# Kernel tuning notes

Measured on AMD Instinct MI355X. Metric: run time of the kernel, lower is better.

Reference implementation:

```python
import jax, jax.numpy as jnp
import numpy as np

N_HEADS = 16
BLOCK_SIZE = 256


def _rope(x):
    # x: [B, H, L, d] ; matches torch RotaryPositionalEmbedding (interleave-split then concat)
    B, H, L, d = x.shape
    inv_freq = 1.0 / (10000.0 ** (jnp.arange(0, d, 2, dtype=jnp.float32) / d))
    t = jnp.arange(L, dtype=jnp.float32)[:, None] * inv_freq[None, :]  # [L, d/2]
    cos, sin = jnp.cos(t), jnp.sin(t)
    x1, x2 = x[..., 0::2], x[..., 1::2]
    return jnp.concatenate([x1 * cos - x2 * sin, x2 * cos + x1 * sin], axis=-1)


def setup_inputs() -> dict:
    key = jax.random.key(0)
    k1, k2, k3 = jax.random.split(key, 3)
    B, L, D = 2, 4096, 1024
    x = jax.random.normal(k1, (B, L, D), dtype=jnp.float32)
    Wqkv = jax.random.normal(k2, (3 * D, D), dtype=jnp.float32) * 0.02
    Wout = jax.random.normal(k3, (D, D), dtype=jnp.float32) * 0.02
    return {"x": x, "Wqkv": Wqkv, "Wout": Wout}


def reference(x, Wqkv, Wout):
    H, BS = N_HEADS, BLOCK_SIZE
    B, L, D = x.shape
    HD = D // H
    scale = HD ** (-0.5)
    nb = L // BS

    qkv = (x @ Wqkv.T).reshape(B, L, 3, H, HD).transpose(2, 0, 3, 1, 4)  # [3,B,H,L,HD]
    q, k, v = qkv[0], qkv[1], qkv[2]
    q, k = _rope(q), _rope(k)

    # block-diagonal causal attention: only within-block scores are ever unmasked,
    # and fp32 exp(finfo.min - max) == 0, so blockwise softmax == masked full softmax
    qb = q.reshape(B, H, nb, BS, HD)
    kb = k.reshape(B, H, nb, BS, HD)
    vb = v.reshape(B, H, nb, BS, HD)

    att = jnp.einsum('bhnqd,bhnkd->bhnqk', qb, kb) * scale
    causal = jnp.tril(jnp.ones((BS, BS), dtype=bool))
    att = jnp.where(causal, att, jnp.finfo(att.dtype).min)
    att = jax.nn.softmax(att, axis=-1)  # dropout p=0.0 -> identity

    out = jnp.einsum('bhnqk,bhnkd->bhnqd', att, vb)
    out = out.reshape(B, H, L, HD).transpose(0, 2, 1, 3).reshape(B, L, D)
    return out @ Wout.T
```

## Files before the change

kernel.cpp:

```cpp
#include <hip/hip_runtime.h>
#include <hip/hip_bf16.h>
#include <cstdint>
#include <cstddef>

typedef __hip_bfloat16 bf16;
typedef __attribute__((ext_vector_type(8))) short bf16x8;
typedef __attribute__((ext_vector_type(4))) float floatx4;

static constexpr int Bb = 2;
static constexpr int Ls = 4096;
static constexpr int Dm = 1024;
static constexpr int Hn = 16;
static constexpr int HD = 64;
static constexpr int BS = 256;
static constexpr int QKVROW = 3 * Dm;
static constexpr int KRP = 72;

static constexpr size_t NX  = (size_t)8192 * 1024;
static constexpr size_t NQ  = (size_t)8192 * 3072;
static constexpr size_t NW1 = (size_t)3072 * 1024;
static constexpr size_t NW2 = (size_t)1024 * 1024;

__device__ __forceinline__ void async_load16(const void* g, void* l) {
  __builtin_amdgcn_global_load_lds(
      (__attribute__((address_space(1))) void*)(void*)(g),
      (__attribute__((address_space(3))) void*)(l), 16, 0, 0);
}

__device__ __forceinline__ short f2bf(float f) {
  union { __hip_bfloat16 b; short s; } u;
  u.b = __float2bfloat16(f);
  return u.s;
}

__device__ __forceinline__ float bf2f(short s) {
  union { unsigned u; float f; } v;
  v.u = ((unsigned)(unsigned short)s) << 16;
  return v.f;
}

__device__ __forceinline__ bf16x8 load8(const float* p) {
  const float4 f0 = *(const float4*)(const void*)p;
  const float4 f1 = *(const float4*)(const void*)(p + 4);
  bf16x8 r;
  r[0] = f2bf(f0.x); r[1] = f2bf(f0.y); r[2] = f2bf(f0.z); r[3] = f2bf(f0.w);
  r[4] = f2bf(f1.x); r[5] = f2bf(f1.y); r[6] = f2bf(f1.z); r[7] = f2bf(f1.w);
  return r;
}

__device__ __forceinline__ void storeC(bf16* C, size_t idx, float v) {
  C[idx] = __float2bfloat16(v);
}
__device__ __forceinline__ void storeC(float* C, size_t idx, float v) {
  C[idx] = v;
}

__global__ void cvt3_kernel(const float* __restrict__ x, const float* __restrict__ w1,
                            const float* __restrict__ w2, bf16* __restrict__ xb,
                            bf16* __restrict__ w1b, bf16* __restrict__ w2b) {
  const size_t i = ((size_t)blockIdx.x * 256 + threadIdx.x) * 8;
  if (i < NX) {
    *(bf16x8*)(void*)((short*)(void*)xb + i) = load8(x + i);
  } else if (i < NX + NW1) {
    const size_t k = i - NX;
    *(bf16x8*)(void*)((short*)(void*)w1b + k) = load8(w1 + k);
  } else {
    const size_t k = i - NX - NW1;
    *(bf16x8*)(void*)((short*)(void*)w2b + k) = load8(w2 + k);
  }
}

template <typename TC>
__global__ __launch_bounds__(512, 2) void gemm_sq(
    const bf16* __restrict__ A, const bf16* __restrict__ Bm, TC* __restrict__ C,
    int M, int N, int K) {
  constexpr int BK = 64;
  __shared__ __align__(16) short sA[2][2][128 * 64];
  __shared__ __align__(16) short sB[2][2][128 * 64];
  const int tid = threadIdx.x;
  const int wave = tid >> 6, lane = tid & 63;
  const int quad = lane >> 4, l15 = lane & 15;
  const int wr = wave >> 2, wc = wave & 3;
  const int tm = blockIdx.y * 256, tn = blockIdx.x * 256;

  const int iLo = tid >> 3;
  const int csP = tid & 7;
  const int csL = csP ^ (iLo & 7);
  const bf16* gA[2][2];
  const bf16* gB[2][2];
#pragma unroll
  for (int h = 0; h < 2; h++)
#pragma unroll
    for (int j = 0; j < 2; j++) {
      gA[h][j] = A + (size_t)(tm + h * 128 + iLo + 64 * j) * K + csL * 8;
      gB[h][j] = Bm + (size_t)(tn + h * 128 + iLo + 64 * j) * K + csL * 8;
    }

#define STGA(buf, h, kb)                                       \
  do {                                                         \
    short* d_ = &sA[buf][h][0] + tid * 8;                      \
    async_load16(gA[h][0] + (kb), d_);                         \
    async_load16(gA[h][1] + (kb), d_ + 4096);                  \
  } while (0)
#define STGB(buf, h, kb)                                       \
  do {                                                         \
    short* d_ = &sB[buf][h][0] + tid * 8;                      \
    async_load16(gB[h][0] + (kb), d_);                         \
    async_load16(gB[h][1] + (kb), d_ + 4096);                  \
  } while (0)
#define BARR()                                                 \
  do {                                                         \
    asm volatile("" ::: "memory");                             \
    __builtin_amdgcn_s_barrier();                              \
    asm volatile("" ::: "memory");                             \
  } while (0)
#define LGKM0() asm volatile("s_waitcnt lgkmcnt(0)" ::: "memory")
#define RDB8(buf)                                                              \
  do {                                                                         \
    const short* p_ = &sB[buf][wc >> 1][0];                                    \
    _Pragma("unroll") for (int n = 0; n < 4; n++)                              \
        _Pragma("unroll") for (int ks = 0; ks < 2; ks++)                       \
            bfr[n][ks] = *(const bf16x8*)(                                     \
                p_ + ((wc & 1) * 64 + n * 16 + l15) * 64                       \
                + (((ks * 4 + quad) ^ (l15 & 7)) * 8));                        \
  } while (0)
#define RDA4(buf, q)                                                           \
  do {                                                                         \
    const short* p_ = &sA[buf][wr][0];                                         \
    _Pragma("unroll") for (int mm = 0; mm < 2; mm++)                           \
        _Pragma("unroll") for (int ks = 0; ks < 2; ks++)                       \
            af[mm][ks] = *(const bf16x8*)(                                     \
                p_ + ((q) * 32 + mm * 16 + l15) * 64                           \
                + (((ks * 4 + quad) ^ (l15 & 7)) * 8));                        \
  } while (0)
#define MM16(q)                                                                \
  do {                                                                         \
    __builtin_amdgcn_s_setprio(1);                                             \
    _Pragma("unroll") for (int mm = 0; mm < 2; mm++)                           \
        _Pragma("unroll") for (int n = 0; n < 4; n++) {                        \
      acc[(q)*2 + mm][n] = __builtin_amdgcn_mfma_f32_16x16x32_bf16(            \
          af[mm][0], bfr[n][0], acc[(q)*2 + mm][n], 0, 0, 0);                  \
      acc[(q)*2 + mm][n] = __builtin_amdgcn_mfma_f32_16x16x32_bf16(            \
          af[mm][1], bfr[n][1], acc[(q)*2 + mm][n], 0, 0, 0);                  \
    }                                                                          \
    __builtin_amdgcn_s_setprio(0);                                             \
  } while (0)

  floatx4 acc[8][4];
#pragma unroll
  for (int i = 0; i < 8; i++)
#pragma unroll
    for (int j = 0; j < 4; j++) acc[i][j] = {0.f, 0.f, 0.f, 0.f};
  bf16x8 af[2][2], bfr[4][2];

  const int nk = K / BK;

  STGA(0, 0, 0);
  STGA(0, 1, 0);
  STGB(0, 0, 0);
  STGB(0, 1, 0);
  STGB(1, 0, BK);
  STGB(1, 1, BK);
  asm volatile("s_waitcnt vmcnt(4)" ::: "memory");
  BARR();

  for (int T = 0; T < nk; ++T) {
    const int buf = T & 1, nbuf = buf ^ 1;
    const int kA = (T + 1) * BK, kB = (T + 2) * BK;
    const bool stA = (T + 1) < nk, stB = (T + 2) < nk;
    RDB8(buf);
    RDA4(buf, 0);
    if (stA) STGA(nbuf, 0, kA);
    asm volatile("s_waitcnt lgkmcnt(8)" ::: "memory");
    BARR();
    LGKM0();
    MM16(0);
    BARR();
    RDA4(buf, 1);
    if (stA) STGA(nbuf, 1, kA);
    BARR();
    LGKM0();
    MM16(1);
    BARR();
    RDA4(buf, 2);
    if (stB) STGB(buf, 0, kB);
    BARR();
    LGKM0();
    MM16(2);
    BARR();
    RDA4(buf, 3);
    if (stB) {
      STGB(buf, 1, kB);
      asm volatile("s_waitcnt vmcnt(4)" ::: "memory");
    } else if (stA) {
      asm volatile("s_waitcnt vmcnt(0)" ::: "memory");
    }
    BARR();
    LGKM0();
    MM16(3);
    BARR();
  }
#undef STGA
#undef STGB
#undef BARR
#undef LGKM0
#undef RDB8
#undef RDA4
#undef MM16

#pragma unroll
  for (int mq = 0; mq < 8; mq++)
#pragma unroll
    for (int n = 0; n < 4; n++)
#pragma unroll
      for (int r = 0; r < 4; r++) {
        const int row = tm + wr * 128 + mq * 16 + quad * 4 + r;
        const int col = tn + wc * 64 + n * 16 + l15;
        storeC(C, (size_t)row * N + col, acc[mq][n][r]);
      }
}

template <typename TC>
__global__ __launch_bounds__(512, 2) void gemm_8p(
    const bf16* __restrict__ A, const bf16* __restrict__ Bm, TC* __restrict__ C,
    int M, int N, int K) {
  constexpr int BK = 64;
  __shared__ __align__(16) short sA[3][256 * 64];
  __shared__ __align__(16) short sB[3][128 * 64];
  const int tid = threadIdx.x;
  const int wave = tid >> 6, lane = tid & 63;
  const int quad = lane >> 4, l15 = lane & 15;
  const int wr = wave >> 1, wc = wave & 1;
  const int tm = blockIdx.y * 256, tn = blockIdx.x * 128;

  const int iLo = tid >> 3;
  const int csP = tid & 7;
  const int csL = csP ^ (iLo & 7);
  const bf16* gA[4];
  const bf16* gB[2];
#pragma unroll
  for (int j = 0; j < 4; j++) gA[j] = A + (size_t)(tm + iLo + 64 * j) * K + csL * 8;
#pragma unroll
  for (int j = 0; j < 2; j++) gB[j] = Bm + (size_t)(tn + iLo + 64 * j) * K + csL * 8;

  short* aC  = &sA[0][0];
  short* aN1 = &sA[1][0];
  short* aN2 = &sA[2][0];
  short* bC  = &sB[0][0];
  short* bN1 = &sB[1][0];
  short* bN2 = &sB[2][0];

#define STH1(aD, bD, kb)                                   \
  do {                                                     \
    async_load16(gA[0] + (kb), (aD) + tid * 8);            \
    async_load16(gA[1] + (kb), (aD) + 4096 + tid * 8);     \
    async_load16(gB[0] + (kb), (bD) + tid * 8);            \
  } while (0)
#define STH2(aD, bD, kb)                                   \
  do {                                                     \
    async_load16(gA[2] + (kb), (aD) + 8192 + tid * 8);     \
    async_load16(gA[3] + (kb), (aD) + 12288 + tid * 8);    \
    async_load16(gB[1] + (kb), (bD) + 4096 + tid * 8);     \
  } while (0)
#define BARR()                                             \
  do {                                                     \
    asm volatile("" ::: "memory");                         \
    __builtin_amdgcn_s_barrier();                          \
    asm volatile("" ::: "memory");                         \
  } while (0)
#define LGKM0() asm volatile("s_waitcnt lgkmcnt(0)" ::: "memory")
#define RDB4(bP)                                                               \
  do {                                                                         \
    _Pragma("unroll") for (int n = 0; n < 4; n++)                              \
        _Pragma("unroll") for (int ks = 0; ks < 2; ks++)                       \
            bfr[n][ks] = *(const bf16x8*)((bP) + (wc * 64 + n * 16 + l15) * 64 \
                              + ((ks * 4 + quad) ^ (l15 & 7)) * 8);            \
  } while (0)
#define RDA2(aP, mh)                                                           \
  do {                                                                         \
    _Pragma("unroll") for (int mm = 0; mm < 2; mm++)                           \
        _Pragma("unroll") for (int ks = 0; ks < 2; ks++)                       \
            af[mm][ks] = *(const bf16x8*)(                                     \
                (aP) + (wr * 64 + ((mh)*2 + mm) * 16 + l15) * 64               \
                + ((ks * 4 + quad) ^ (l15 & 7)) * 8);                          \
  } while (0)
#define MM16(mh)                                                               \
  do {                                                                         \
    __builtin_amdgcn_s_setprio(1);                                             \
    _Pragma("unroll") for (int mm = 0; mm < 2; mm++)                           \
        _Pragma("unroll") for (int n = 0; n < 4; n++) {                        \
      acc[(mh)*2 + mm][n] = __builtin_amdgcn_mfma_f32_16x16x32_bf16(           \
          af[mm][0], bfr[n][0], acc[(mh)*2 + mm][n], 0, 0, 0);                 \
      acc[(mh)*2 + mm][n] = __builtin_amdgcn_mfma_f32_16x16x32_bf16(           \
          af[mm][1], bfr[n][1], acc[(mh)*2 + mm][n], 0, 0, 0);                 \
    }                                                                          \
    __builtin_amdgcn_s_setprio(0);                                             \
  } while (0)

  floatx4 acc[4][4];
#pragma unroll
  for (int i = 0; i < 4; i++)
#pragma unroll
    for (int j = 0; j < 4; j++) acc[i][j] = {0.f, 0.f, 0.f, 0.f};
  bf16x8 af[2][2], bfr[4][2];

  const int nk = K / BK;

  STH1(aC, bC, 0);
  STH2(aC, bC, 0);
  STH1(aN1, bN1, BK);
  STH2(aN1, bN1, BK);
  asm volatile("s_waitcnt vmcnt(6)" ::: "memory");
  BARR();

  for (int t = 0; t < nk - 2; ++t) {
    const int kb2 = (t + 2) * BK;
    RDB4(bC);
    RDA2(aC, 0);
    STH1(aN2, bN2, kb2);
    BARR();
    LGKM0();
    MM16(0);
    BARR();
    RDA2(aC, 1);
    STH2(aN2, bN2, kb2);
    asm volatile("s_waitcnt vmcnt(6)" ::: "memory");
    BARR();
    LGKM0();
    MM16(1);
    BARR();
    short* ta = aC; aC = aN1; aN1 = aN2; aN2 = ta;
    short* tb = bC; bC = bN1; bN1 = bN2; bN2 = tb;
  }
  RDB4(bC);
  RDA2(aC, 0);
  BARR();
  LGKM0();
  MM16(0);
  BARR();
  RDA2(aC, 1);
  asm volatile("s_waitcnt vmcnt(0)" ::: "memory");
  BARR();
  LGKM0();
  MM16(1);
  BARR();
  {
    short* ta = aC; aC = aN1; aN1 = aN2; aN2 = ta;
    short* tb = bC; bC = bN1; bN1 = bN2; bN2 = tb;
  }
  RDB4(bC);
  RDA2(aC, 0);
  LGKM0();
  MM16(0);
  RDA2(aC, 1);
  LGKM0();
  MM16(1);
#undef STH1
#undef STH2
#undef BARR
#undef LGKM0
#undef RDB4
#undef RDA2
#undef MM16

#pragma unroll
  for (int m = 0; m < 4; m++)
#pragma unroll
    for (int n = 0; n < 4; n++)
#pragma unroll
      for (int r = 0; r < 4; r++) {
        const int row = tm + wr * 64 + m * 16 + quad * 4 + r;
        const int col = tn + wc * 64 + n * 16 + l15;
        storeC(C, (size_t)row * N + col, acc[m][n][r]);
      }
}

__device__ __forceinline__ void rope_frag(const bf16* __restrict__ row, int quad,
                                          float l_pos, const float* __restrict__ freq8,
                                          bf16x8* f0, bf16x8* f1) {
  const bf16x8 w0 = *(const bf16x8*)(const void*)(row + quad * 16);
  const bf16x8 w1 = *(const bf16x8*)(const void*)(row + quad * 16 + 8);
#pragma unroll
  for (int j = 0; j < 8; j++) {
    const short s1 = (j < 4) ? w0[2 * j] : w1[2 * (j - 4)];
    const short s2 = (j < 4) ? w0[2 * j + 1] : w1[2 * (j - 4) + 1];
    const float x1 = bf2f(s1), x2 = bf2f(s2);
    const float rev = l_pos * freq8[j];
    const float fr = rev - floorf(rev);
    const float c = __builtin_amdgcn_cosf(fr);
    const float s = __builtin_amdgcn_sinf(fr);
    (*f0)[j] = f2bf(x1 * c - x2 * s);
    (*f1)[j] = f2bf(x2 * c + x1 * s);
  }
}

__global__ __launch_bounds__(256) void attn_kernel(const bf16* __restrict__ qkv,
                                                   bf16* __restrict__ aout) {
  constexpr float SCALE = 0.125f;
  constexpr float LOG2E = 1.4426950408889634f;
  constexpr float INV2PI = 0.15915494309189535f;
  __shared__ __align__(16) short vT[HD * BS];
  __shared__ __align__(16) short kR[BS * KRP];
  __shared__ __align__(16) short pS[4][16 * 64];
  const int blk = blockIdx.x, h = blockIdx.y, b = blockIdx.z;
  const int tid = threadIdx.x;
  const int wave = tid >> 6, lane = tid & 63;
  const int quad = lane >> 4, l15 = lane & 15;
  const size_t row0 = (size_t)(b * Ls + blk * BS);
  const bf16* qkvR = qkv + row0 * QKVROW;

  float freq8[8];
#pragma unroll
  for (int j = 0; j < 8; j++)
    freq8[j] = exp2f(-13.287712379549449f * (float)(2 * (quad * 8 + j)) * (1.0f / 64.0f))
               * INV2PI;

  {
    const bf16* vrow = qkvR + (size_t)tid * QKVROW + 2 * Dm + h * HD;
#pragma unroll
    for (int i = 0; i < 8; i++) {
      bf16x8 vv = *(const bf16x8*)(vrow + i * 8);
#pragma unroll
      for (int e = 0; e < 8; e++) vT[(i * 8 + e) * BS + tid] = vv[e];
    }
  }

  {
    const bf16* krow = qkvR + (size_t)tid * QKVROW + Dm + h * HD;
    bf16x8 kw[8];
#pragma unroll
    for (int t = 0; t < 8; t++) kw[t] = *(const bf16x8*)(krow + t * 8);
    const float pos = (float)(blk * BS + tid);
    short tmp[64];
#pragma unroll
    for (int i = 0; i < 32; i++) {
      const float x1 = bf2f(kw[(2 * i) >> 3][(2 * i) & 7]);
      const float x2 = bf2f(kw[(2 * i + 1) >> 3][(2 * i + 1) & 7]);
      const float fq = exp2f(-13.287712379549449f * (float)(2 * i) * (1.0f / 64.0f)) * INV2PI;
      const float rev = pos * fq;
      const float fr = rev - floorf(rev);
      const float c = __builtin_amdgcn_cosf(fr);
      const float s = __builtin_amdgcn_sinf(fr);
      tmp[i]      = f2bf(x1 * c - x2 * s);
      tmp[i + 32] = f2bf(x2 * c + x1 * s);
    }
#pragma unroll
    for (int t = 0; t < 8; t++)
      *(bf16x8*)(kR + tid * KRP + t * 8) = *(const bf16x8*)(tmp + t * 8);
  }
  __syncthreads();

  short* myP = &pS[wave][0];

  for (int sp = 0; sp < 2; sp++) {
    const int s = sp ? (7 - wave) : wave;
    const int qrow0 = s * 32;
    const int kcmax = s >> 1;

    bf16x8 qf[2][2];
#pragma unroll
    for (int mt = 0; mt < 2; mt++) {
      const int qr = qrow0 + mt * 16 + l15;
      rope_frag(qkvR + (size_t)qr * QKVROW + h * HD, quad,
                (float)(blk * BS + qr), freq8, &qf[mt][0], &qf[mt][1]);
    }

    float m_i[2][4], l_i[2][4];
    floatx4 o[2][4];
#pragma unroll
    for (int mt = 0; mt < 2; mt++)
#pragma unroll
      for (int r = 0; r < 4; r++) { m_i[mt][r] = -1e30f; l_i[mt][r] = 0.f; }
#pragma unroll
    for (int mt = 0; mt < 2; mt++)
#pragma unroll
      for (int nt = 0; nt < 4; nt++) o[mt][nt] = {0.f, 0.f, 0.f, 0.f};

    for (int kc = 0; kc <= kcmax; kc++) {
      floatx4 sc[2][4];
#pragma unroll
      for (int mt = 0; mt < 2; mt++)
#pragma unroll
        for (int nt = 0; nt < 4; nt++) sc[mt][nt] = {0.f, 0.f, 0.f, 0.f};

      bf16x8 kf[4][2];
#pragma unroll
      for (int nt = 0; nt < 4; nt++) {
        const short* kr = kR + (kc * 64 + nt * 16 + l15) * KRP;
        kf[nt][0] = *(const bf16x8*)(kr + quad * 8);
        kf[nt][1] = *(const bf16x8*)(kr + 32 + quad * 8);
      }

#pragma unroll
      for (int mt = 0; mt < 2; mt++)
#pragma unroll
        for (int nt = 0; nt < 4; nt++) {
          sc[mt][nt] = __builtin_amdgcn_mfma_f32_16x16x32_bf16(qf[mt][0], kf[nt][0], sc[mt][nt], 0, 0, 0);
          sc[mt][nt] = __builtin_amdgcn_mfma_f32_16x16x32_bf16(qf[mt][1], kf[nt][1], sc[mt][nt], 0, 0, 0);
        }

      const bool diag = (kc == kcmax);
#pragma unroll
      for (int mt = 0; mt < 2; mt++)
#pragma unroll
        for (int r = 0; r < 4; r++) {
          const int rowg = qrow0 + mt * 16 + quad * 4 + r;
          float cmax = -1e30f;
#pragma unroll
          for (int nt = 0; nt < 4; nt++) {
            float sv = sc[mt][nt][r] * SCALE;
            if (diag && (kc * 64 + nt * 16 + l15 > rowg)) sv = -1e30f;
            sc[mt][nt][r] = sv;
            cmax = fmaxf(cmax, sv);
          }
#pragma unroll
          for (int off = 1; off < 16; off <<= 1)
            cmax = fmaxf(cmax, __shfl_xor(cmax, off, 64));
          const float mold = m_i[mt][r];
          const float mnew = fmaxf(mold, cmax);
          const float alpha = exp2f((mold - mnew) * LOG2E);
          float rsum = 0.f;
#pragma unroll
          for (int nt = 0; nt < 4; nt++) {
            const float p = exp2f((sc[mt][nt][r] - mnew) * LOG2E);
            sc[mt][nt][r] = p;
            rsum += p;
          }
#pragma unroll
          for (int off = 1; off < 16; off <<= 1)
            rsum += __shfl_xor(rsum, off, 64);
          l_i[mt][r] = l_i[mt][r] * alpha + rsum;
          m_i[mt][r] = mnew;
#pragma unroll
          for (int nt = 0; nt < 4; nt++) o[mt][nt][r] *= alpha;
        }

      bf16x8 vf0[4], vf1[4];
#pragma unroll
      for (int nt = 0; nt < 4; nt++) {
        vf0[nt] = *(const bf16x8*)(vT + (nt * 16 + l15) * BS + kc * 64 + quad * 8);
        vf1[nt] = *(const bf16x8*)(vT + (nt * 16 + l15) * BS + kc * 64 + 32 + quad * 8);
      }

#pragma unroll
      for (int mt = 0; mt < 2; mt++) {
#pragma unroll
        for (int nt = 0; nt < 4; nt++)
#pragma unroll
          for (int r = 0; r < 4; r++)
            myP[(quad * 4 + r) * 64 + nt * 16 + l15] = f2bf(sc[mt][nt][r]);
        __asm__ __volatile__("s_waitcnt lgkmcnt(0)" ::: "memory");
        const bf16x8 pf0 = *(const bf16x8*)(myP + l15 * 64 + quad * 8);
        const bf16x8 pf1 = *(const bf16x8*)(myP + l15 * 64 + 32 + quad * 8);
#pragma unroll
        for (int nt = 0; nt < 4; nt++) {
          o[mt][nt] = __builtin_amdgcn_mfma_f32_16x16x32_bf16(pf0, vf0[nt], o[mt][nt], 0, 0, 0);
          o[mt][nt] = __builtin_amdgcn_mfma_f32_16x16x32_bf16(pf1, vf1[nt], o[mt][nt], 0, 0, 0);
        }
        __asm__ __volatile__("s_waitcnt lgkmcnt(0)" ::: "memory");
      }
    }

#pragma unroll
    for (int mt = 0; mt < 2; mt++)
#pragma unroll
      for (int r = 0; r < 4; r++) {
        const float inv = 1.0f / l_i[mt][r];
#pragma unroll
        for (int nt = 0; nt < 4; nt++) {
          const size_t m = row0 + qrow0 + mt * 16 + quad * 4 + r;
          aout[m * Dm + h * HD + nt * 16 + l15] = __float2bfloat16(o[mt][nt][r] * inv);
        }
      }
  }
}

extern "C" void kernel_launch(void* const* d_in, const int* in_sizes, int n_in,
                              void* d_out, int out_size, void* d_ws, size_t ws_size,
                              hipStream_t stream) {
  const float* x    = (const float*)d_in[0];
  const float* Wqkv = (const float*)d_in[1];
  const float* Wout = (const float*)d_in[2];
  float* out = (float*)d_out;

  bf16* xb    = (bf16*)d_ws;
  bf16* qkv   = xb + NX;
  bf16* Wqkvb = qkv + NQ;
  bf16* Woutb = Wqkvb + NW1;
  bf16* attnb = xb;

  cvt3_kernel<<<(NX + NW1 + NW2) / 2048, 256, 0, stream>>>(x, Wqkv, Wout, xb, Wqkvb, Woutb);

  gemm_sq<bf16>
      <<<dim3(3072 / 256, 8192 / 256), 512, 0, stream>>>(xb, Wqkvb, qkv, 8192, 3072, 1024);
  attn_kernel<<<dim3(Ls / BS, Hn, Bb), 256, 0, stream>>>(qkv, attnb);
  gemm_8p<float>
      <<<dim3(1024 / 128, 8192 / 256), 512, 0, stream>>>(attnb, Woutb, out, 8192, 1024, 1024);
}
```

Before: 221.2 us.

## Use 256x192 tiles with XCD-aware block swizzle for QKV GEMM

Changes the QKV projection GEMM tile from 256x256 to 256x192, which gives 512 blocks (a multiple of the CU count) instead of 384, and so evens out wave quantization. A 1D grid with a swizzle groups consecutive tiles per XCD for better L2 reuse. The B staging is merged into one three-load step and the waitcnt counts are adjusted. Per-block arithmetic intensity drops slightly and the pipeline accounting changes.

```diff
diff --git a/kernel.cpp b/kernel.cpp
--- a/kernel.cpp
+++ b/kernel.cpp
@@ -71,42 +71,49 @@
 }
 
 template <typename TC>
-__global__ __launch_bounds__(512, 2) void gemm_sq(
+__global__ __launch_bounds__(512, 2) void gemm_192(
     const bf16* __restrict__ A, const bf16* __restrict__ Bm, TC* __restrict__ C,
     int M, int N, int K) {
   constexpr int BK = 64;
-  __shared__ __align__(16) short sA[2][2][128 * 64];
-  __shared__ __align__(16) short sB[2][2][128 * 64];
+  __shared__ __align__(16) short sA[2][256 * 64];
+  __shared__ __align__(16) short sB[2][192 * 64];
   const int tid = threadIdx.x;
   const int wave = tid >> 6, lane = tid & 63;
   const int quad = lane >> 4, l15 = lane & 15;
   const int wr = wave >> 2, wc = wave & 3;
-  const int tm = blockIdx.y * 256, tn = blockIdx.x * 256;
+  const int nt = N / 192;
+  const int cpx = gridDim.x >> 3;
+  const int lid = blockIdx.x;
+  const int swz = (lid & 7) * cpx + (lid >> 3);
+  const int tm = (swz / nt) * 256;
+  const int tn = (swz % nt) * 192;
 
   const int iLo = tid >> 3;
   const int csP = tid & 7;
   const int csL = csP ^ (iLo & 7);
   const bf16* gA[2][2];
-  const bf16* gB[2][2];
+  const bf16* gB[3];
 #pragma unroll
   for (int h = 0; h < 2; h++)
 #pragma unroll
-    for (int j = 0; j < 2; j++) {
+    for (int j = 0; j < 2; j++)
       gA[h][j] = A + (size_t)(tm + h * 128 + iLo + 64 * j) * K + csL * 8;
-      gB[h][j] = Bm + (size_t)(tn + h * 128 + iLo + 64 * j) * K + csL * 8;
-    }
+#pragma unroll
+  for (int j = 0; j < 3; j++)
+    gB[j] = Bm + (size_t)(tn + iLo + 64 * j) * K + csL * 8;
 
 #define STGA(buf, h, kb)                                       \
   do {                                                         \
-    short* d_ = &sA[buf][h][0] + tid * 8;                      \
+    short* d_ = &sA[buf][0] + (h) * 8192 + tid * 8;            \
     async_load16(gA[h][0] + (kb), d_);                         \
     async_load16(gA[h][1] + (kb), d_ + 4096);                  \
   } while (0)
-#define STGB(buf, h, kb)                                       \
+#define STGB(buf, kb)                                          \
   do {                                                         \
-    short* d_ = &sB[buf][h][0] + tid * 8;                      \
-    async_load16(gB[h][0] + (kb), d_);                         \
-    async_load16(gB[h][1] + (kb), d_ + 4096);                  \
+    short* d_ = &sB[buf][0] + tid * 8;                         \
+    async_load16(gB[0] + (kb), d_);                            \
+    async_load16(gB[1] + (kb), d_ + 4096);                     \
+    async_load16(gB[2] + (kb), d_ + 8192);                     \
   } while (0)
 #define BARR()                                                 \
   do {                                                         \
@@ -115,29 +122,29 @@
     asm volatile("" ::: "memory");                             \
   } while (0)
 #define LGKM0() asm volatile("s_waitcnt lgkmcnt(0)" ::: "memory")
-#define RDB8(buf)                                                              \
+#define RDB6(buf)                                                              \
   do {                                                                         \
-    const short* p_ = &sB[buf][wc >> 1][0];                                    \
-    _Pragma("unroll") for (int n = 0; n < 4; n++)                              \
+    const short* p_ = &sB[buf][0];                                             \
+    _Pragma("unroll") for (int n = 0; n < 3; n++)                              \
         _Pragma("unroll") for (int ks = 0; ks < 2; ks++)                       \
             bfr[n][ks] = *(const bf16x8*)(                                     \
-                p_ + ((wc & 1) * 64 + n * 16 + l15) * 64                       \
+                p_ + (wc * 48 + n * 16 + l15) * 64                             \
                 + (((ks * 4 + quad) ^ (l15 & 7)) * 8));                        \
   } while (0)
 #define RDA4(buf, q)                                                           \
   do {                                                                         \
-    const short* p_ = &sA[buf][wr][0];                                         \
+    const short* p_ = &sA[buf][0];                                             \
     _Pragma("unroll") for (int mm = 0; mm < 2; mm++)                           \
         _Pragma("unroll") for (int ks = 0; ks < 2; ks++)                       \
             af[mm][ks] = *(const bf16x8*)(                                     \
-                p_ + ((q) * 32 + mm * 16 + l15) * 64                           \
+                p_ + (wr * 128 + (q) * 32 + mm * 16 + l15) * 64                \
                 + (((ks * 4 + quad) ^ (l15 & 7)) * 8));                        \
   } while (0)
-#define MM16(q)                                                                \
+#define MM12(q)                                                                \
   do {                                                                         \
     __builtin_amdgcn_s_setprio(1);                                             \
     _Pragma("unroll") for (int mm = 0; mm < 2; mm++)                           \
-        _Pragma("unroll") for (int n = 0; n < 4; n++) {                        \
+        _Pragma("unroll") for (int n = 0; n < 3; n++) {                        \
       acc[(q)*2 + mm][n] = __builtin_amdgcn_mfma_f32_16x16x32_bf16(            \
           af[mm][0], bfr[n][0], acc[(q)*2 + mm][n], 0, 0, 0);                  \
       acc[(q)*2 + mm][n] = __builtin_amdgcn_mfma_f32_16x16x32_bf16(            \
@@ -146,76 +153,72 @@
     __builtin_amdgcn_s_setprio(0);                                             \
   } while (0)
 
-  floatx4 acc[8][4];
+  floatx4 acc[8][3];
 #pragma unroll
   for (int i = 0; i < 8; i++)
 #pragma unroll
-    for (int j = 0; j < 4; j++) acc[i][j] = {0.f, 0.f, 0.f, 0.f};
-  bf16x8 af[2][2], bfr[4][2];
+    for (int j = 0; j < 3; j++) acc[i][j] = {0.f, 0.f, 0.f, 0.f};
+  bf16x8 af[2][2], bfr[3][2];
 
   const int nk = K / BK;
 
   STGA(0, 0, 0);
   STGA(0, 1, 0);
-  STGB(0, 0, 0);
-  STGB(0, 1, 0);
-  STGB(1, 0, BK);
-  STGB(1, 1, BK);
-  asm volatile("s_waitcnt vmcnt(4)" ::: "memory");
+  STGB(0, 0);
+  STGB(1, BK);
+  asm volatile("s_waitcnt vmcnt(3)" ::: "memory");
   BARR();
 
   for (int T = 0; T < nk; ++T) {
     const int buf = T & 1, nbuf = buf ^ 1;
     const int kA = (T + 1) * BK, kB = (T + 2) * BK;
     const bool stA = (T + 1) < nk, stB = (T + 2) < nk;
-    RDB8(buf);
+    RDB6(buf);
     RDA4(buf, 0);
     if (stA) STGA(nbuf, 0, kA);
-    asm volatile("s_waitcnt lgkmcnt(8)" ::: "memory");
     BARR();
     LGKM0();
-    MM16(0);
+    MM12(0);
     BARR();
     RDA4(buf, 1);
     if (stA) STGA(nbuf, 1, kA);
     BARR();
     LGKM0();
-    MM16(1);
+    MM12(1);
     BARR();
     RDA4(buf, 2);
-    if (stB) STGB(buf, 0, kB);
+    if (stB) STGB(buf, kB);
     BARR();
     LGKM0();
-    MM16(2);
+    MM12(2);
     BARR();
     RDA4(buf, 3);
     if (stB) {
-      STGB(buf, 1, kB);
-      asm volatile("s_waitcnt vmcnt(4)" ::: "memory");
+      asm volatile("s_waitcnt vmcnt(3)" ::: "memory");
     } else if (stA) {
       asm volatile("s_waitcnt vmcnt(0)" ::: "memory");
     }
     BARR();
     LGKM0();
-    MM16(3);
+    MM12(3);
     BARR();
   }
 #undef STGA
 #undef STGB
 #undef BARR
 #undef LGKM0
-#undef RDB8
+#undef RDB6
 #undef RDA4
-#undef MM16
+#undef MM12
 
 #pragma unroll
   for (int mq = 0; mq < 8; mq++)
 #pragma unroll
-    for (int n = 0; n < 4; n++)
+    for (int n = 0; n < 3; n++)
 #pragma unroll
       for (int r = 0; r < 4; r++) {
         const int row = tm + wr * 128 + mq * 16 + quad * 4 + r;
-        const int col = tn + wc * 64 + n * 16 + l15;
+        const int col = tn + wc * 48 + n * 16 + l15;
         storeC(C, (size_t)row * N + col, acc[mq][n][r]);
       }
 }
@@ -591,8 +594,8 @@
 
   cvt3_kernel<<<(NX + NW1 + NW2) / 2048, 256, 0, stream>>>(x, Wqkv, Wout, xb, Wqkvb, Woutb);
 
-  gemm_sq<bf16>
-      <<<dim3(3072 / 256, 8192 / 256), 512, 0, stream>>>(xb, Wqkvb, qkv, 8192, 3072, 1024);
+  gemm_192<bf16>
+      <<<512, 512, 0, stream>>>(xb, Wqkvb, qkv, 8192, 3072, 1024);
   attn_kernel<<<dim3(Ls / BS, Hn, Bb), 256, 0, stream>>>(qkv, attnb);
   gemm_8p<float>
       <<<dim3(1024 / 128, 8192 / 256), 512, 0, stream>>>(attnb, Woutb, out, 8192, 1024, 1024);
```

New measurement: 220.9 us. About the same (-0.1%).

## Software-pipeline LDS fragment reads in 256x128 GEMM and split QKV GEMM

Applied to the files above, without the earlier changes.

Reworks the 256x128 GEMM main loop so the B fragments and first A half-fragments for the next K tile are read from LDS while the current tile's MFMAs run. It uses double-buffered register fragments and partial lgkmcnt waits in place of full drains. The QKV projection is split into two launches: the square-tile kernel covers the Q/K columns and the pipelined kernel covers the V columns through a new column-offset parameter. The cost is more registers, more complex wait-count logic, and an extra kernel launch.

```diff
diff --git a/kernel.cpp b/kernel.cpp
--- a/kernel.cpp
+++ b/kernel.cpp
@@ -73,7 +73,7 @@
 template <typename TC>
 __global__ __launch_bounds__(512, 2) void gemm_sq(
     const bf16* __restrict__ A, const bf16* __restrict__ Bm, TC* __restrict__ C,
-    int M, int N, int K) {
+    int M, int N, int K, int nOff) {
   constexpr int BK = 64;
   __shared__ __align__(16) short sA[2][2][128 * 64];
   __shared__ __align__(16) short sB[2][2][128 * 64];
@@ -81,7 +81,7 @@
   const int wave = tid >> 6, lane = tid & 63;
   const int quad = lane >> 4, l15 = lane & 15;
   const int wr = wave >> 2, wc = wave & 3;
-  const int tm = blockIdx.y * 256, tn = blockIdx.x * 256;
+  const int tm = blockIdx.y * 256, tn = blockIdx.x * 256 + nOff;
 
   const int iLo = tid >> 3;
   const int csP = tid & 7;
@@ -221,9 +221,9 @@
 }
 
 template <typename TC>
-__global__ __launch_bounds__(512, 2) void gemm_8p(
+__global__ __launch_bounds__(512, 2) void gemm_pl(
     const bf16* __restrict__ A, const bf16* __restrict__ Bm, TC* __restrict__ C,
-    int M, int N, int K) {
+    int M, int N, int K, int nOff) {
   constexpr int BK = 64;
   __shared__ __align__(16) short sA[3][256 * 64];
   __shared__ __align__(16) short sB[3][128 * 64];
@@ -231,7 +231,7 @@
   const int wave = tid >> 6, lane = tid & 63;
   const int quad = lane >> 4, l15 = lane & 15;
   const int wr = wave >> 1, wc = wave & 1;
-  const int tm = blockIdx.y * 256, tn = blockIdx.x * 128;
+  const int tm = blockIdx.y * 256, tn = blockIdx.x * 128 + nOff;
 
   const int iLo = tid >> 3;
   const int csP = tid & 7;
@@ -268,41 +268,67 @@
     __builtin_amdgcn_s_barrier();                          \
     asm volatile("" ::: "memory");                         \
   } while (0)
-#define LGKM0() asm volatile("s_waitcnt lgkmcnt(0)" ::: "memory")
-#define RDB4(bP)                                                               \
+#define RDB8(bP, DST)                                                          \
   do {                                                                         \
     _Pragma("unroll") for (int n = 0; n < 4; n++)                              \
         _Pragma("unroll") for (int ks = 0; ks < 2; ks++)                       \
-            bfr[n][ks] = *(const bf16x8*)((bP) + (wc * 64 + n * 16 + l15) * 64 \
+            DST[n][ks] = *(const bf16x8*)((bP) + (wc * 64 + n * 16 + l15) * 64 \
                               + ((ks * 4 + quad) ^ (l15 & 7)) * 8);            \
   } while (0)
-#define RDA2(aP, mh)                                                           \
+#define RDA2(aP, DST, mh)                                                      \
   do {                                                                         \
     _Pragma("unroll") for (int mm = 0; mm < 2; mm++)                           \
         _Pragma("unroll") for (int ks = 0; ks < 2; ks++)                       \
-            af[mm][ks] = *(const bf16x8*)(                                     \
+            DST[mm][ks] = *(const bf16x8*)(                                    \
                 (aP) + (wr * 64 + ((mh)*2 + mm) * 16 + l15) * 64               \
                 + ((ks * 4 + quad) ^ (l15 & 7)) * 8);                          \
   } while (0)
-#define MM16(mh)                                                               \
+#define MM16(AF, BF, mh)                                                       \
   do {                                                                         \
     __builtin_amdgcn_s_setprio(1);                                             \
     _Pragma("unroll") for (int mm = 0; mm < 2; mm++)                           \
         _Pragma("unroll") for (int n = 0; n < 4; n++) {                        \
       acc[(mh)*2 + mm][n] = __builtin_amdgcn_mfma_f32_16x16x32_bf16(           \
-          af[mm][0], bfr[n][0], acc[(mh)*2 + mm][n], 0, 0, 0);                 \
+          AF[mm][0], BF[n][0], acc[(mh)*2 + mm][n], 0, 0, 0);                  \
       acc[(mh)*2 + mm][n] = __builtin_amdgcn_mfma_f32_16x16x32_bf16(           \
-          af[mm][1], bfr[n][1], acc[(mh)*2 + mm][n], 0, 0, 0);                 \
+          AF[mm][1], BF[n][1], acc[(mh)*2 + mm][n], 0, 0, 0);                  \
     }                                                                          \
     __builtin_amdgcn_s_setprio(0);                                             \
   } while (0)
+#define TILE(t, BCUR, BNXT)                                                    \
+  do {                                                                         \
+                                                                  \
+    RDA2(aC, afH, 1);                                                          \
+    if ((t) + 2 < nk) STH1(aN2, bN2, ((t) + 2) * BK);                          \
+    if ((t) + 2 < nk)                                                          \
+      asm volatile("s_waitcnt vmcnt(3)" ::: "memory");                         \
+    else if ((t) + 1 < nk)                                                     \
+      asm volatile("s_waitcnt vmcnt(0)" ::: "memory");                         \
+    BARR();                                                                    \
+    asm volatile("s_waitcnt lgkmcnt(4)" ::: "memory");                         \
+    MM16(afL, BCUR, 0);                                                        \
+    BARR();                                                                    \
+                                                                  \
+    if ((t) + 1 < nk) {                                                        \
+      RDB8(bN1, BNXT);                                                         \
+      RDA2(aN1, afL, 0);                                                       \
+      if ((t) + 2 < nk) STH2(aN2, bN2, ((t) + 2) * BK);                        \
+      asm volatile("s_waitcnt lgkmcnt(12)" ::: "memory");                      \
+    } else {                                                                   \
+      asm volatile("s_waitcnt lgkmcnt(0)" ::: "memory");                       \
+    }                                                                          \
+    MM16(afH, BCUR, 1);                                                        \
+    BARR();                                                                    \
+    { short* ta_ = aC; aC = aN1; aN1 = aN2; aN2 = ta_; }                       \
+    { short* tb_ = bC; bC = bN1; bN1 = bN2; bN2 = tb_; }                       \
+  } while (0)
 
   floatx4 acc[4][4];
 #pragma unroll
   for (int i = 0; i < 4; i++)
 #pragma unroll
     for (int j = 0; j < 4; j++) acc[i][j] = {0.f, 0.f, 0.f, 0.f};
-  bf16x8 af[2][2], bfr[4][2];
+  bf16x8 afL[2][2], afH[2][2], bfrA[4][2], bfrB[4][2];
 
   const int nk = K / BK;
 
@@ -312,56 +338,20 @@
   STH2(aN1, bN1, BK);
   asm volatile("s_waitcnt vmcnt(6)" ::: "memory");
   BARR();
-
-  for (int t = 0; t < nk - 2; ++t) {
-    const int kb2 = (t + 2) * BK;
-    RDB4(bC);
-    RDA2(aC, 0);
-    STH1(aN2, bN2, kb2);
-    BARR();
-    LGKM0();
-    MM16(0);
-    BARR();
-    RDA2(aC, 1);
-    STH2(aN2, bN2, kb2);
-    asm volatile("s_waitcnt vmcnt(6)" ::: "memory");
-    BARR();
-    LGKM0();
-    MM16(1);
-    BARR();
-    short* ta = aC; aC = aN1; aN1 = aN2; aN2 = ta;
-    short* tb = bC; bC = bN1; bN1 = bN2; bN2 = tb;
-  }
-  RDB4(bC);
-  RDA2(aC, 0);
-  BARR();
-  LGKM0();
-  MM16(0);
-  BARR();
-  RDA2(aC, 1);
-  asm volatile("s_waitcnt vmcnt(0)" ::: "memory");
-  BARR();
-  LGKM0();
-  MM16(1);
-  BARR();
-  {
-    short* ta = aC; aC = aN1; aN1 = aN2; aN2 = ta;
-    short* tb = bC; bC = bN1; bN1 = bN2; bN2 = tb;
-  }
-  RDB4(bC);
-  RDA2(aC, 0);
-  LGKM0();
-  MM16(0);
-  RDA2(aC, 1);
-  LGKM0();
-  MM16(1);
+  RDB8(bC, bfrA);
+  RDA2(aC, afL, 0);
+
+  for (int t = 0; t < nk; t += 2) {
+    TILE(t, bfrA, bfrB);
+    TILE(t + 1, bfrB, bfrA);
+  }
 #undef STH1
 #undef STH2
 #undef BARR
-#undef LGKM0
-#undef RDB4
+#undef RDB8
 #undef RDA2
 #undef MM16
+#undef TILE
 
 #pragma unroll
   for (int m = 0; m < 4; m++)
@@ -592,8 +582,10 @@
   cvt3_kernel<<<(NX + NW1 + NW2) / 2048, 256, 0, stream>>>(x, Wqkv, Wout, xb, Wqkvb, Woutb);
 
   gemm_sq<bf16>
-      <<<dim3(3072 / 256, 8192 / 256), 512, 0, stream>>>(xb, Wqkvb, qkv, 8192, 3072, 1024);
+      <<<dim3(2048 / 256, 8192 / 256), 512, 0, stream>>>(xb, Wqkvb, qkv, 8192, 3072, 1024, 0);
+  gemm_pl<bf16>
+      <<<dim3(1024 / 128, 8192 / 256), 512, 0, stream>>>(xb, Wqkvb, qkv, 8192, 3072, 1024, 2048);
   attn_kernel<<<dim3(Ls / BS, Hn, Bb), 256, 0, stream>>>(qkv, attnb);
-  gemm_8p<float>
-      <<<dim3(1024 / 128, 8192 / 256), 512, 0, stream>>>(attnb, Woutb, out, 8192, 1024, 1024);
-}
+  gemm_pl<float>
+      <<<dim3(1024 / 128, 8192 / 256), 512, 0, stream>>>(attnb, Woutb, out, 8192, 1024, 1024, 0);
+}
```

New measurement: 219.5 us. Within noise of the previous version (-0.7%).
